# Kernel tuning notes

Hardware: AMD Instinct MI355X
Metric: run time of the kernel (lower is better)

Reference implementation:

```python
import jax, jax.numpy as jnp
import numpy as np

GAMMA = 0.5

def smooth_step(t, gamma=GAMMA):
    # DSelect-k SmoothStep: 0 below -g/2, 1 above g/2, cubic in between.
    tc = jnp.clip(t, -gamma / 2, gamma / 2)
    return (-2.0 / gamma**3) * tc**3 + (3.0 / (2.0 * gamma)) * tc + 0.5

def setup_inputs() -> dict:
    key = jax.random.key(0)
    k1, k2, k3 = jax.random.split(key, 3)
    B, p, k, m = 65536, 1024, 8, 6
    x = jax.random.normal(k1, (B, p), dtype=jnp.float32)
    G_w = jax.random.normal(k2, (k, p), dtype=jnp.float32) / np.sqrt(p)
    G_b = jnp.zeros((k,), dtype=jnp.float32)
    W_w = jax.random.normal(k3, (k * m, p), dtype=jnp.float32) / np.sqrt(p)
    W_b = jnp.zeros((k * m,), dtype=jnp.float32)
    return {"x": x, "G_w": G_w, "G_b": G_b, "W_w": W_w, "W_b": W_b}

def reference(x, G_w, G_b, W_w, W_b):
    B = x.shape[0]
    k = G_w.shape[0]
    m = W_w.shape[0] // k
    n = 2 ** m  # number of experts encoded by m binary gates
    gates = (x @ W_w.T + W_b).reshape(B, k, m)
    z = smooth_step(gates)  # (B, k, m) in [0, 1]
    # per_example_selector: probability of expert e = prod_j (z_j if bit_j(e) else 1-z_j)
    bits = ((np.arange(n)[:, None] >> np.arange(m)[None, :]) & 1).astype(bool)  # (n, m)
    bits = jnp.asarray(bits)
    sel = jnp.prod(jnp.where(bits[None, None, :, :], z[:, :, None, :], 1.0 - z[:, :, None, :]), axis=-1)  # (B, k, n)
    weights = jax.nn.softmax(x @ G_w.T + G_b, axis=1)  # (B, k)
    mixture = jnp.einsum('bk,bkn->bn', weights, sel)  # bmm((B,1,k),(B,k,n)) -> (B, n)
    return mixture
```

## Files before the change

kernel.cpp:

```cpp
#include <hip/hip_runtime.h>

typedef _Float16 half8 __attribute__((ext_vector_type(8)));
typedef float f32x4 __attribute__((ext_vector_type(4)));
typedef float f4 __attribute__((ext_vector_type(4)));

#define P_DIM 1024
#define BM 64
#define NH 8
#define AF_ROW 132

__global__ __launch_bounds__(256) void prep_weights(
    const float* __restrict__ Gw, const float* __restrict__ Gb,
    const float* __restrict__ Ww, const float* __restrict__ Wb,
    _Float16* __restrict__ Wf2, float* __restrict__ biasC) {
  int i = blockIdx.x * 256 + threadIdx.x;
  int j = i & 7;
  int l = (i >> 3) & 63;
  int t = (i >> 9) & 3;
  int S = i >> 11;
  int row = t * 16 + (l & 15);
  int k   = S * 32 + (l >> 4) * 8 + j;
  float v = 0.0f;
  if (row < 48) v = Ww[row * P_DIM + k];
  else if (row < 56) v = Gw[(row - 48) * P_DIM + k];
  Wf2[i] = (_Float16)v;
  if (i < 64) {
    float bv = 0.0f;
    if (i < 48) bv = Wb[i];
    else if (i < 56) bv = Gb[i - 48];
    biasC[i] = bv;
  }
}

#define LOAD_B(dst, c) do { const char* p_ = bgw + (size_t)(c) * 8192; \
    dst[0] = *(const half8*)(p_);          dst[1] = *(const half8*)(p_ + 4096); \
    dst[2] = *(const half8*)(p_ + 1024);   dst[3] = *(const half8*)(p_ + 5120); \
  } while (0)

#define BODY(bX, cc) do { \
    f4 a0_[4], a1_[4]; \
    { const char* p0 = Abase0 + (cc) * 256; \
      a0_[0] = *(const f4*)(p0);       a0_[1] = *(const f4*)(p0 + 16); \
      a0_[2] = *(const f4*)(p0 + 128); a0_[3] = *(const f4*)(p0 + 144); \
      const char* p1 = Abase1 + (cc) * 256; \
      a1_[0] = *(const f4*)(p1);       a1_[1] = *(const f4*)(p1 + 16); \
      a1_[2] = *(const f4*)(p1 + 128); a1_[3] = *(const f4*)(p1 + 144); } \
    half8 h00_, h01_, h10_, h11_; \
    h00_[0]=(_Float16)a0_[0][0]; h00_[1]=(_Float16)a0_[0][1]; h00_[2]=(_Float16)a0_[0][2]; h00_[3]=(_Float16)a0_[0][3]; \
    h00_[4]=(_Float16)a0_[1][0]; h00_[5]=(_Float16)a0_[1][1]; h00_[6]=(_Float16)a0_[1][2]; h00_[7]=(_Float16)a0_[1][3]; \
    h01_[0]=(_Float16)a0_[2][0]; h01_[1]=(_Float16)a0_[2][1]; h01_[2]=(_Float16)a0_[2][2]; h01_[3]=(_Float16)a0_[2][3]; \
    h01_[4]=(_Float16)a0_[3][0]; h01_[5]=(_Float16)a0_[3][1]; h01_[6]=(_Float16)a0_[3][2]; h01_[7]=(_Float16)a0_[3][3]; \
    h10_[0]=(_Float16)a1_[0][0]; h10_[1]=(_Float16)a1_[0][1]; h10_[2]=(_Float16)a1_[0][2]; h10_[3]=(_Float16)a1_[0][3]; \
    h10_[4]=(_Float16)a1_[1][0]; h10_[5]=(_Float16)a1_[1][1]; h10_[6]=(_Float16)a1_[1][2]; h10_[7]=(_Float16)a1_[1][3]; \
    h11_[0]=(_Float16)a1_[2][0]; h11_[1]=(_Float16)a1_[2][1]; h11_[2]=(_Float16)a1_[2][2]; h11_[3]=(_Float16)a1_[2][3]; \
    h11_[4]=(_Float16)a1_[3][0]; h11_[5]=(_Float16)a1_[3][1]; h11_[6]=(_Float16)a1_[3][2]; h11_[7]=(_Float16)a1_[3][3]; \
    acc[0] = __builtin_amdgcn_mfma_f32_16x16x32_f16(h00_, bX[0], acc[0], 0, 0, 0); \
    acc[0] = __builtin_amdgcn_mfma_f32_16x16x32_f16(h01_, bX[1], acc[0], 0, 0, 0); \
    acc[1] = __builtin_amdgcn_mfma_f32_16x16x32_f16(h00_, bX[2], acc[1], 0, 0, 0); \
    acc[1] = __builtin_amdgcn_mfma_f32_16x16x32_f16(h01_, bX[3], acc[1], 0, 0, 0); \
    acc[2] = __builtin_amdgcn_mfma_f32_16x16x32_f16(h10_, bX[0], acc[2], 0, 0, 0); \
    acc[2] = __builtin_amdgcn_mfma_f32_16x16x32_f16(h11_, bX[1], acc[2], 0, 0, 0); \
    acc[3] = __builtin_amdgcn_mfma_f32_16x16x32_f16(h10_, bX[2], acc[3], 0, 0, 0); \
    acc[3] = __builtin_amdgcn_mfma_f32_16x16x32_f16(h11_, bX[3], acc[3], 0, 0, 0); \
  } while (0)

__global__ __launch_bounds__(256, 3) void fused_gate(
    const float* __restrict__ x, const _Float16* __restrict__ Wf2,
    const float* __restrict__ biasC, float* __restrict__ out) {
  __shared__ __align__(16) float Af[BM][AF_ROW];

  const int tid  = threadIdx.x;
  const int lane = tid & 63;
  const int w    = tid >> 6;
  const int row0 = blockIdx.x * BM;
  const int l15  = lane & 15;
  const int q    = lane >> 4;

  const int mrow = (w >> 1) * 32;
  const int ncol = (w & 1) * 32;

  const char* xg = (const char*)(x + (size_t)(row0 + w * 16) * P_DIM) + lane * 8;
  const char* bgw = (const char*)Wf2 + lane * 16 + (size_t)(ncol / 16) * 1024;

  char* Aw = (char*)&Af[w * 16][0] + lane * 8;
  const char* Abase0 = (const char*)&Af[mrow + l15][0] + q * 32;
  const char* Abase1 = Abase0 + 16 * 528;

  f32x4 acc[4];
#pragma unroll
  for (int t = 0; t < 4; ++t) acc[t] = (f32x4){0.f, 0.f, 0.f, 0.f};

  float2 pf[16];
#pragma unroll
  for (int i = 0; i < 16; ++i) pf[i] = *(const float2*)(xg + i * 4096);

  half8 bA[4], bB[4];
  LOAD_B(bA, 0);

  for (int h = 0; h < NH; ++h) {
    if (h) __syncthreads();
#pragma unroll
    for (int i = 0; i < 16; ++i)
      *(float2*)(Aw + i * 528) = pf[i];
    __syncthreads();
    const int c0 = h * 2;
    LOAD_B(bB, c0 + 1);
    if (h + 1 < NH) {
#pragma unroll
      for (int i = 0; i < 16; ++i)
        pf[i] = *(const float2*)(xg + i * 4096 + (h + 1) * 512);
    }
    BODY(bA, 0);
    BODY(bB, 1);
    if (h + 1 < NH)
      LOAD_B(bA, c0 + 2);
  }

  __syncthreads();
  float (*S)[65] = (float (*)[65])&Af[0][0];

#pragma unroll
  for (int m = 0; m < 2; ++m) {
#pragma unroll
    for (int j = 0; j < 2; ++j) {
      const int col = ncol + j * 16 + l15;
      float bias = biasC[col];
#pragma unroll
      for (int rr = 0; rr < 4; ++rr) {
        S[mrow + m * 16 + q * 4 + rr][col] = acc[m * 2 + j][rr] + bias;
      }
    }
  }
  __syncthreads();

  const int r2  = tid >> 2;
  const int sub = tid & 3;

  float lg[8];
#pragma unroll
  for (int k = 0; k < 8; ++k) lg[k] = S[r2][48 + k];
  float mx = lg[0];
#pragma unroll
  for (int k = 1; k < 8; ++k) mx = fmaxf(mx, lg[k]);
  float wk[8];
  float ssum = 0.f;
#pragma unroll
  for (int k = 0; k < 8; ++k) { wk[k] = expf(lg[k] - mx); ssum += wk[k]; }
  const float inv = 1.0f / ssum;

  float mix[16];
#pragma unroll
  for (int i = 0; i < 16; ++i) mix[i] = 0.f;

#pragma unroll
  for (int k = 0; k < 8; ++k) {
    float z[6];
#pragma unroll
    for (int j = 0; j < 6; ++j) {
      float tt = S[r2][k * 6 + j];
      float tc = fminf(fmaxf(tt, -0.25f), 0.25f);
      z[j] = fmaf(tc, fmaf(-16.0f * tc, tc, 3.0f), 0.5f);
    }
    float f4v = (sub & 1) ? z[4] : 1.0f - z[4];
    float f5v = (sub & 2) ? z[5] : 1.0f - z[5];
    float wf = wk[k] * inv * f4v * f5v;
    float t2[2], t4[4], t8[8], t16[16];
    t2[0] = 1.0f - z[0]; t2[1] = z[0];
#pragma unroll
    for (int i = 0; i < 2; ++i) { t4[i] = t2[i] * (1.0f - z[1]); t4[i + 2] = t2[i] * z[1]; }
#pragma unroll
    for (int i = 0; i < 4; ++i) { t8[i] = t4[i] * (1.0f - z[2]); t8[i + 4] = t4[i] * z[2]; }
#pragma unroll
    for (int i = 0; i < 8; ++i) { t16[i] = t8[i] * (1.0f - z[3]); t16[i + 8] = t8[i] * z[3]; }
#pragma unroll
    for (int i = 0; i < 16; ++i) mix[i] = fmaf(wf, t16[i], mix[i]);
  }

  float* op = out + (size_t)(row0 + r2) * 64 + sub * 16;
#pragma unroll
  for (int g = 0; g < 4; ++g) {
    float4 o;
    o.x = mix[4 * g + 0]; o.y = mix[4 * g + 1];
    o.z = mix[4 * g + 2]; o.w = mix[4 * g + 3];
    ((float4*)op)[g] = o;
  }
}

extern "C" void kernel_launch(void* const* d_in, const int* in_sizes, int n_in,
                              void* d_out, int out_size, void* d_ws, size_t ws_size,
                              hipStream_t stream) {
  const float* x  = (const float*)d_in[0];
  const float* Gw = (const float*)d_in[1];
  const float* Gb = (const float*)d_in[2];
  const float* Ww = (const float*)d_in[3];
  const float* Wb = (const float*)d_in[4];
  float* out = (float*)d_out;

  _Float16* Wf2  = (_Float16*)d_ws;
  float*    bias = (float*)((char*)d_ws + 64 * P_DIM * sizeof(_Float16));

  const int B = in_sizes[0] / P_DIM;

  prep_weights<<<dim3(256), dim3(256), 0, stream>>>(Gw, Gb, Ww, Wb, Wf2, bias);
  fused_gate<<<dim3(B / BM), dim3(256), 0, stream>>>(x, Wf2, bias, out);
  (void)n_in; (void)out_size; (void)ws_size;
}
```

Before: 58.43 us.

## Convert x tiles to fp16 before LDS staging and widen K chunk per stage

Converts prefetched x values to fp16 when writing them into shared memory, so the LDS tile holds half-precision data and the MFMA operands are read as single half8 loads with no per-iteration conversion. Global loads are widened to float4 and each stage now covers 256 K columns over 4 stages instead of 128 over 8, halving the number of barriers. The B-operand loads are re-interleaved with four MFMA bodies per stage. This cuts LDS traffic and conversion instructions in the inner loop, at the cost of more live registers for the wider prefetch buffer, which could reduce occupancy.

```diff
diff --git a/kernel.cpp b/kernel.cpp
--- a/kernel.cpp
+++ b/kernel.cpp
@@ -1,13 +1,13 @@
 #include <hip/hip_runtime.h>
 
 typedef _Float16 half8 __attribute__((ext_vector_type(8)));
+typedef _Float16 half4 __attribute__((ext_vector_type(4)));
 typedef float f32x4 __attribute__((ext_vector_type(4)));
-typedef float f4 __attribute__((ext_vector_type(4)));
 
 #define P_DIM 1024
 #define BM 64
-#define NH 8
-#define AF_ROW 132
+#define NS 4
+#define AH_COLS 264
 
 __global__ __launch_bounds__(256) void prep_weights(
     const float* __restrict__ Gw, const float* __restrict__ Gb,
@@ -38,22 +38,10 @@
   } while (0)
 
 #define BODY(bX, cc) do { \
-    f4 a0_[4], a1_[4]; \
-    { const char* p0 = Abase0 + (cc) * 256; \
-      a0_[0] = *(const f4*)(p0);       a0_[1] = *(const f4*)(p0 + 16); \
-      a0_[2] = *(const f4*)(p0 + 128); a0_[3] = *(const f4*)(p0 + 144); \
-      const char* p1 = Abase1 + (cc) * 256; \
-      a1_[0] = *(const f4*)(p1);       a1_[1] = *(const f4*)(p1 + 16); \
-      a1_[2] = *(const f4*)(p1 + 128); a1_[3] = *(const f4*)(p1 + 144); } \
-    half8 h00_, h01_, h10_, h11_; \
-    h00_[0]=(_Float16)a0_[0][0]; h00_[1]=(_Float16)a0_[0][1]; h00_[2]=(_Float16)a0_[0][2]; h00_[3]=(_Float16)a0_[0][3]; \
-    h00_[4]=(_Float16)a0_[1][0]; h00_[5]=(_Float16)a0_[1][1]; h00_[6]=(_Float16)a0_[1][2]; h00_[7]=(_Float16)a0_[1][3]; \
-    h01_[0]=(_Float16)a0_[2][0]; h01_[1]=(_Float16)a0_[2][1]; h01_[2]=(_Float16)a0_[2][2]; h01_[3]=(_Float16)a0_[2][3]; \
-    h01_[4]=(_Float16)a0_[3][0]; h01_[5]=(_Float16)a0_[3][1]; h01_[6]=(_Float16)a0_[3][2]; h01_[7]=(_Float16)a0_[3][3]; \
-    h10_[0]=(_Float16)a1_[0][0]; h10_[1]=(_Float16)a1_[0][1]; h10_[2]=(_Float16)a1_[0][2]; h10_[3]=(_Float16)a1_[0][3]; \
-    h10_[4]=(_Float16)a1_[1][0]; h10_[5]=(_Float16)a1_[1][1]; h10_[6]=(_Float16)a1_[1][2]; h10_[7]=(_Float16)a1_[1][3]; \
-    h11_[0]=(_Float16)a1_[2][0]; h11_[1]=(_Float16)a1_[2][1]; h11_[2]=(_Float16)a1_[2][2]; h11_[3]=(_Float16)a1_[2][3]; \
-    h11_[4]=(_Float16)a1_[3][0]; h11_[5]=(_Float16)a1_[3][1]; h11_[6]=(_Float16)a1_[3][2]; h11_[7]=(_Float16)a1_[3][3]; \
+    half8 h00_ = *(const half8*)(Ab0 + (cc) * 128); \
+    half8 h01_ = *(const half8*)(Ab0 + (cc) * 128 + 64); \
+    half8 h10_ = *(const half8*)(Ab1 + (cc) * 128); \
+    half8 h11_ = *(const half8*)(Ab1 + (cc) * 128 + 64); \
     acc[0] = __builtin_amdgcn_mfma_f32_16x16x32_f16(h00_, bX[0], acc[0], 0, 0, 0); \
     acc[0] = __builtin_amdgcn_mfma_f32_16x16x32_f16(h01_, bX[1], acc[0], 0, 0, 0); \
     acc[1] = __builtin_amdgcn_mfma_f32_16x16x32_f16(h00_, bX[2], acc[1], 0, 0, 0); \
@@ -67,7 +55,7 @@
 __global__ __launch_bounds__(256, 3) void fused_gate(
     const float* __restrict__ x, const _Float16* __restrict__ Wf2,
     const float* __restrict__ biasC, float* __restrict__ out) {
-  __shared__ __align__(16) float Af[BM][AF_ROW];
+  __shared__ __align__(16) _Float16 Ah[BM][AH_COLS];
 
   const int tid  = threadIdx.x;
   const int lane = tid & 63;
@@ -79,45 +67,54 @@
   const int mrow = (w >> 1) * 32;
   const int ncol = (w & 1) * 32;
 
-  const char* xg = (const char*)(x + (size_t)(row0 + w * 16) * P_DIM) + lane * 8;
+  const char* xg = (const char*)(x + (size_t)(row0 + w * 16) * P_DIM) + lane * 16;
   const char* bgw = (const char*)Wf2 + lane * 16 + (size_t)(ncol / 16) * 1024;
 
-  char* Aw = (char*)&Af[w * 16][0] + lane * 8;
-  const char* Abase0 = (const char*)&Af[mrow + l15][0] + q * 32;
-  const char* Abase1 = Abase0 + 16 * 528;
+  char* Aw = (char*)&Ah[w * 16][0] + lane * 8;
+  const char* Ab0 = (const char*)&Ah[mrow + l15][0] + q * 16;
+  const char* Ab1 = Ab0 + 16 * 528;
 
   f32x4 acc[4];
 #pragma unroll
   for (int t = 0; t < 4; ++t) acc[t] = (f32x4){0.f, 0.f, 0.f, 0.f};
-
-  float2 pf[16];
-#pragma unroll
-  for (int i = 0; i < 16; ++i) pf[i] = *(const float2*)(xg + i * 4096);
 
   half8 bA[4], bB[4];
   LOAD_B(bA, 0);
-
-  for (int h = 0; h < NH; ++h) {
-    if (h) __syncthreads();
-#pragma unroll
-    for (int i = 0; i < 16; ++i)
-      *(float2*)(Aw + i * 528) = pf[i];
+  float4 pf[16];
+#pragma unroll
+  for (int i = 0; i < 16; ++i) pf[i] = *(const float4*)(xg + i * 4096);
+
+  for (int s = 0; s < NS; ++s) {
+    if (s) __syncthreads();
+#pragma unroll
+    for (int i = 0; i < 16; ++i) {
+      half4 hv;
+      hv[0] = (_Float16)pf[i].x;
+      hv[1] = (_Float16)pf[i].y;
+      hv[2] = (_Float16)pf[i].z;
+      hv[3] = (_Float16)pf[i].w;
+      *(half4*)(Aw + i * 528) = hv;
+    }
     __syncthreads();
-    const int c0 = h * 2;
+    const int c0 = 4 * s;
     LOAD_B(bB, c0 + 1);
-    if (h + 1 < NH) {
+    BODY(bA, 0);
+    LOAD_B(bA, c0 + 2);
+    if (s + 1 < NS) {
 #pragma unroll
       for (int i = 0; i < 16; ++i)
-        pf[i] = *(const float2*)(xg + i * 4096 + (h + 1) * 512);
-    }
-    BODY(bA, 0);
+        pf[i] = *(const float4*)(xg + i * 4096 + (s + 1) * 1024);
+    }
     BODY(bB, 1);
-    if (h + 1 < NH)
-      LOAD_B(bA, c0 + 2);
+    LOAD_B(bB, c0 + 3);
+    BODY(bA, 2);
+    if (s + 1 < NS)
+      LOAD_B(bA, c0 + 4);
+    BODY(bB, 3);
   }
 
   __syncthreads();
-  float (*S)[65] = (float (*)[65])&Af[0][0];
+  float (*S)[65] = (float (*)[65])&Ah[0][0];
 
 #pragma unroll
   for (int m = 0; m < 2; ++m) {
```

After: 64.65 us. +10.6%, slower.
